# Kernel tuning notes

Hardware: AMD Instinct MI355X
Metric: run time of the kernel (lower is better)

The kernel has to match this reference:

```python
import jax, jax.numpy as jnp
import numpy as np

N = 8_388_608
T_MAX = 4096


def setup_inputs() -> dict:
    key = jax.random.key(0)
    k1, k2, k3 = jax.random.split(key, 3)
    risk = jax.random.normal(k1, (N,), dtype=jnp.float32)
    time = jax.random.randint(k2, (N,), 0, T_MAX, dtype=jnp.int64)
    event = jax.random.randint(k3, (N,), 0, 2, dtype=jnp.int64)
    return {"risk": risk, "time": time, "event": event}


def reference(risk, time, event):
    # Sort descending by time (matches torch.argsort(time, descending=True)).
    order = jnp.argsort(-time)
    r = risk[order]            # [N] risk sorted by descending time
    t = time[order]            # [N]
    e = event[order] > 0       # [N] bool

    n = r.shape[0]
    # Cumulative (prefix) logsumexp over descending-sorted risks.
    # At-risk set for time t is exactly the prefix ending at the LAST index
    # of t's tie group, so log_denom(group) = clse[last_idx_of_group].
    clse = jax.lax.associative_scan(jnp.logaddexp, r)  # [N]

    # Last index of each contiguous tie block (times equal => contiguous after sort).
    is_last = jnp.concatenate([t[:-1] != t[1:], jnp.ones((1,), dtype=bool)])
    idx = jnp.arange(n)
    cand = jnp.where(is_last, idx, n)          # non-last positions -> sentinel
    last_idx = jax.lax.cummin(cand, axis=0, reverse=True)  # min over j >= i

    log_denom = clse[last_idx]                 # [N] per-sample group denominator

    # nll = -sum_groups(sum_{events in group} risk  -  d_group * log_denom)
    #     =  sum_{i: event_i} (log_denom_i - risk_i)
    nll = jnp.sum(jnp.where(e, log_denom - r, jnp.float32(0.0)))

    has_events = jnp.sum(event > 0) > 0
    return jnp.where(has_events, nll, jnp.float32(0.0))
```

## Files before the change

### kernel.cpp

```cpp
#include <hip/hip_runtime.h>

#define TMAX 4096
#define ABLOCKS 256
#define ATHREADS 1024
#define PERTHREAD_V4 8

#define SCALE_F 131072.0f
#define INV_SCALE (1.0 / 131072.0)
#define LSUM_MASK 0x03FFFFFFu
#define LCNT_SHIFT 26
#define LSUM_CAP 67108863.0f

#define SUM_MASK 0xFFFFFFFFFFFFULL
#define CNT_SHIFT 48

#define EVR_SCALE 1048576.0
#define EVR_INV   (1.0 / 1048576.0)

#define PROC1(rv, tv, ev)                                                     \
    do {                                                                      \
        const float xs = fminf(__expf(rv) * SCALE_F + 0.5f, LSUM_CAP);        \
        const unsigned pk = (unsigned)xs                                      \
            | ((unsigned)(ev) << LCNT_SHIFT);                                 \
        atomicAdd(&s_acc[(tv) & (TMAX - 1)], pk);                             \
        evr = __builtin_fmaf((float)(ev), (rv), evr);                         \
    } while (0)

#define PROC4(rr, tt, ee)                                                     \
    do {                                                                      \
        PROC1((rr).x, (tt).x, (ee).x);                                        \
        PROC1((rr).y, (tt).y, (ee).y);                                        \
        PROC1((rr).z, (tt).z, (ee).z);                                        \
        PROC1((rr).w, (tt).w, (ee).w);                                        \
    } while (0)

__global__ __launch_bounds__(ATHREADS, 4) void coxph_fused(
    const float* __restrict__ risk, const int* __restrict__ time_,
    const int* __restrict__ event,
    unsigned long long* __restrict__ gaccR,
    unsigned long long* __restrict__ evracc,
    unsigned* __restrict__ done, float* __restrict__ out)
{
    __shared__ unsigned s_acc[TMAX];
    __shared__ float s_evr[ATHREADS / 64];
    __shared__ unsigned s_old;

    const int tid = threadIdx.x;
    #pragma unroll
    for (int k = 0; k < TMAX / ATHREADS; ++k) s_acc[tid + k * ATHREADS] = 0u;
    __syncthreads();

    const float4* r4 = (const float4*)risk;
    const int4*   t4 = (const int4*)time_;
    const int4*   e4 = (const int4*)event;

    const int base = blockIdx.x * ATHREADS + tid;
    const int S4   = ABLOCKS * ATHREADS;

    float evr = 0.f;

    float4 rA, rB; int4 tA, tB, eA, eB;
#define LOADA(k) do { const int i = base + (k) * S4; rA = r4[i]; tA = t4[i]; eA = e4[i]; } while (0)
#define LOADB(k) do { const int i = base + (k) * S4; rB = r4[i]; tB = t4[i]; eB = e4[i]; } while (0)

    LOADA(0); LOADB(1);
    PROC4(rA, tA, eA); LOADA(2);
    PROC4(rB, tB, eB); LOADB(3);
    PROC4(rA, tA, eA); LOADA(4);
    PROC4(rB, tB, eB); LOADB(5);
    PROC4(rA, tA, eA); LOADA(6);
    PROC4(rB, tB, eB); LOADB(7);
    PROC4(rA, tA, eA);
    PROC4(rB, tB, eB);
#undef LOADA
#undef LOADB

    #pragma unroll
    for (int off = 32; off > 0; off >>= 1) evr += __shfl_down(evr, off);
    const int lane = tid & 63, wave = tid >> 6;
    if (lane == 0) s_evr[wave] = evr;
    __syncthreads();

    #pragma unroll
    for (int k = 0; k < TMAX / ATHREADS; ++k) {
        const int i = tid + k * ATHREADS;
        const unsigned v = s_acc[i];
        if (v) {
            const unsigned long long pk =
                (unsigned long long)(v & LSUM_MASK)
                | ((unsigned long long)(v >> LCNT_SHIFT) << CNT_SHIFT);
            atomicAdd(&gaccR[TMAX - 1 - i], pk);
        }
    }
    if (tid == 0) {
        float tot = 0.f;
        for (int w = 0; w < ATHREADS / 64; ++w) tot += s_evr[w];
        const long long q = (long long)llrint((double)tot * EVR_SCALE);
        atomicAdd(evracc, (unsigned long long)q);
    }

    __syncthreads();
    if (tid == 0) s_old = atomicAdd(done, 1u);
    __syncthreads();
    if (s_old != (unsigned)(ABLOCKS - 1)) return;

    __shared__ float    s_wsum[16];
    __shared__ double   s_dacc[16];
    __shared__ unsigned s_cacc[16];

    const int j0 = 4 * tid;
    const unsigned long long gx = atomicAdd(&gaccR[j0 + 0], 0ull);
    const unsigned long long gy = atomicAdd(&gaccR[j0 + 1], 0ull);
    const unsigned long long gz = atomicAdd(&gaccR[j0 + 2], 0ull);
    const unsigned long long gw = atomicAdd(&gaccR[j0 + 3], 0ull);

    const float v0 = (float)((double)(gx & SUM_MASK) * INV_SCALE);
    const float v1 = (float)((double)(gy & SUM_MASK) * INV_SCALE);
    const float v2 = (float)((double)(gz & SUM_MASK) * INV_SCALE);
    const float v3 = (float)((double)(gw & SUM_MASK) * INV_SCALE);
    const unsigned c0 = (unsigned)(gx >> CNT_SHIFT);
    const unsigned c1 = (unsigned)(gy >> CNT_SHIFT);
    const unsigned c2 = (unsigned)(gz >> CNT_SHIFT);
    const unsigned c3 = (unsigned)(gw >> CNT_SHIFT);

    const float p0 = v0, p1 = p0 + v1, p2 = p1 + v2, p3 = p2 + v3;

    float t_incl = p3;
    #pragma unroll
    for (int off = 1; off < 64; off <<= 1) {
        float u = __shfl_up(t_incl, off);
        if (lane >= off) t_incl += u;
    }
    if (lane == 63) s_wsum[wave] = t_incl;
    __syncthreads();
    if (tid == 0) {
        float a = 0.f;
        for (int w = 0; w < 16; ++w) { float x = s_wsum[w]; s_wsum[w] = a; a += x; }
    }
    __syncthreads();
    const float excl = (t_incl - p3) + s_wsum[wave];

    double acc = 0.0; unsigned ctot = 0u;
    if (c0) { acc += (double)c0 * (double)logf(excl + p0); ctot += c0; }
    if (c1) { acc += (double)c1 * (double)logf(excl + p1); ctot += c1; }
    if (c2) { acc += (double)c2 * (double)logf(excl + p2); ctot += c2; }
    if (c3) { acc += (double)c3 * (double)logf(excl + p3); ctot += c3; }

    if (tid == 0) {
        const long long q = (long long)atomicAdd(evracc, 0ull);
        acc -= (double)q * EVR_INV;
    }

    #pragma unroll
    for (int off = 32; off > 0; off >>= 1) {
        acc  += __shfl_down(acc, off);
        ctot += __shfl_down(ctot, off);
    }
    if (lane == 0) { s_dacc[wave] = acc; s_cacc[wave] = ctot; }
    __syncthreads();
    if (tid == 0) {
        double a = 0.0; unsigned cc = 0u;
        for (int w = 0; w < 16; ++w) { a += s_dacc[w]; cc += s_cacc[w]; }
        out[0] = cc ? (float)a : 0.0f;
    }
}

__global__ __launch_bounds__(ATHREADS, 4) void coxph_hist_generic(
    const float* __restrict__ risk, const int* __restrict__ time_,
    const int* __restrict__ event,
    unsigned long long* __restrict__ gaccR, float* __restrict__ pevr, int n)
{
    __shared__ unsigned long long s_acc[TMAX];
    __shared__ float s_evr[ATHREADS / 64];

    const int tid = threadIdx.x;
    #pragma unroll
    for (int k = 0; k < TMAX / ATHREADS; ++k) s_acc[tid + k * ATHREADS] = 0ull;
    __syncthreads();

    float evr = 0.f;
    const int stride = gridDim.x * ATHREADS;
    for (int i = blockIdx.x * ATHREADS + tid; i < n; i += stride) {
        const float rv = risk[i];
        const int   ev = event[i];
        const int   tv = time_[i];
        const unsigned long long pk =
            (unsigned long long)(unsigned)(__expf(rv) * SCALE_F + 0.5f)
            | ((unsigned long long)(unsigned)ev << CNT_SHIFT);
        atomicAdd(&s_acc[tv & (TMAX - 1)], pk);
        evr = __builtin_fmaf((float)ev, rv, evr);
    }

    #pragma unroll
    for (int off = 32; off > 0; off >>= 1) evr += __shfl_down(evr, off);
    const int lane = tid & 63, wave = tid >> 6;
    if (lane == 0) s_evr[wave] = evr;
    __syncthreads();

    #pragma unroll
    for (int k = 0; k < TMAX / ATHREADS; ++k) {
        const int i = tid + k * ATHREADS;
        const unsigned long long v = s_acc[i];
        if (v) atomicAdd(&gaccR[TMAX - 1 - i], v);
    }
    if (tid == 0) {
        float tot = 0.f;
        for (int w = 0; w < ATHREADS / 64; ++w) tot += s_evr[w];
        pevr[blockIdx.x] = tot;
    }
}

__global__ __launch_bounds__(1024) void coxph_finalize(
    const unsigned long long* __restrict__ gaccR,
    const float* __restrict__ pevr, int nevr, float* __restrict__ out)
{
    __shared__ float    s_wsum[16];
    __shared__ double   s_dacc[16];
    __shared__ unsigned s_cacc[16];

    const int tid = threadIdx.x;
    const int lane = tid & 63, wave = tid >> 6;

    const ulonglong4 g = ((const ulonglong4*)gaccR)[tid];
    const float v0 = (float)((double)(g.x & SUM_MASK) * INV_SCALE);
    const float v1 = (float)((double)(g.y & SUM_MASK) * INV_SCALE);
    const float v2 = (float)((double)(g.z & SUM_MASK) * INV_SCALE);
    const float v3 = (float)((double)(g.w & SUM_MASK) * INV_SCALE);
    const unsigned c0 = (unsigned)(g.x >> CNT_SHIFT);
    const unsigned c1 = (unsigned)(g.y >> CNT_SHIFT);
    const unsigned c2 = (unsigned)(g.z >> CNT_SHIFT);
    const unsigned c3 = (unsigned)(g.w >> CNT_SHIFT);

    const float p0 = v0, p1 = p0 + v1, p2 = p1 + v2, p3 = p2 + v3;

    float t_incl = p3;
    #pragma unroll
    for (int off = 1; off < 64; off <<= 1) {
        float u = __shfl_up(t_incl, off);
        if (lane >= off) t_incl += u;
    }
    if (lane == 63) s_wsum[wave] = t_incl;
    __syncthreads();
    if (tid == 0) {
        float a = 0.f;
        for (int w = 0; w < 16; ++w) { float x = s_wsum[w]; s_wsum[w] = a; a += x; }
    }
    __syncthreads();
    const float excl = (t_incl - p3) + s_wsum[wave];

    double acc = 0.0; unsigned ctot = 0u;
    if (c0) { acc += (double)c0 * (double)logf(excl + p0); ctot += c0; }
    if (c1) { acc += (double)c1 * (double)logf(excl + p1); ctot += c1; }
    if (c2) { acc += (double)c2 * (double)logf(excl + p2); ctot += c2; }
    if (c3) { acc += (double)c3 * (double)logf(excl + p3); ctot += c3; }

    if (tid < nevr) acc -= (double)pevr[tid];

    #pragma unroll
    for (int off = 32; off > 0; off >>= 1) {
        acc  += __shfl_down(acc, off);
        ctot += __shfl_down(ctot, off);
    }
    if (lane == 0) { s_dacc[wave] = acc; s_cacc[wave] = ctot; }
    __syncthreads();
    if (tid == 0) {
        double a = 0.0; unsigned cc = 0u;
        for (int w = 0; w < 16; ++w) { a += s_dacc[w]; cc += s_cacc[w]; }
        out[0] = cc ? (float)a : 0.0f;
    }
}

extern "C" void kernel_launch(void* const* d_in, const int* in_sizes, int n_in,
                              void* d_out, int out_size, void* d_ws, size_t ws_size,
                              hipStream_t stream)
{
    const float* risk  = (const float*)d_in[0];
    const int*   time_ = (const int*)d_in[1];
    const int*   event = (const int*)d_in[2];
    float* out = (float*)d_out;
    const int n = in_sizes[0];

    char* ws = (char*)d_ws;
    unsigned long long* gaccR  = (unsigned long long*)ws;
    unsigned long long* evracc = (unsigned long long*)(ws + TMAX * 8);
    unsigned*           done   = (unsigned*)(ws + TMAX * 8 + 8);
    float*              pevr   = (float*)(ws + TMAX * 8 + 16);

    (void)hipMemsetAsync(ws, 0, TMAX * 8 + 16, stream);

    if (n == ABLOCKS * ATHREADS * 4 * PERTHREAD_V4) {
        coxph_fused<<<ABLOCKS, ATHREADS, 0, stream>>>(
            risk, time_, event, gaccR, evracc, done, out);
    } else {
        coxph_hist_generic<<<ABLOCKS, ATHREADS, 0, stream>>>(
            risk, time_, event, gaccR, pevr, n);
        coxph_finalize<<<1, 1024, 0, stream>>>(gaccR, pevr, ABLOCKS, out);
    }
}
```

Before: 124.2 us.

## Use atomic ticket-based dynamic chunk scheduling in fused CoxPH histogram kernel

```diff
diff --git a/kernel.cpp b/kernel.cpp
--- a/kernel.cpp
+++ b/kernel.cpp
@@ -4,6 +4,9 @@
 #define ABLOCKS 256
 #define ATHREADS 1024
 #define PERTHREAD_V4 8
+
+#define NCHUNK  1024
+#define CHUNKV4 2048
 
 #define SCALE_F 131072.0f
 #define INV_SCALE (1.0 / 131072.0)
@@ -39,46 +42,52 @@
     const int* __restrict__ event,
     unsigned long long* __restrict__ gaccR,
     unsigned long long* __restrict__ evracc,
-    unsigned* __restrict__ done, float* __restrict__ out)
+    unsigned* __restrict__ done, unsigned* __restrict__ ticket,
+    float* __restrict__ out)
 {
     __shared__ unsigned s_acc[TMAX];
-    __shared__ float s_evr[ATHREADS / 64];
+    __shared__ long long s_evrq[ATHREADS / 64];
+    __shared__ unsigned s_chunkbuf[2];
     __shared__ unsigned s_old;
 
     const int tid = threadIdx.x;
+    const int lane = tid & 63, wave = tid >> 6;
+
     #pragma unroll
     for (int k = 0; k < TMAX / ATHREADS; ++k) s_acc[tid + k * ATHREADS] = 0u;
+
+    if (tid == 0) s_chunkbuf[0] = atomicAdd(ticket, 1u);
     __syncthreads();
 
     const float4* r4 = (const float4*)risk;
     const int4*   t4 = (const int4*)time_;
     const int4*   e4 = (const int4*)event;
 
-    const int base = blockIdx.x * ATHREADS + tid;
-    const int S4   = ABLOCKS * ATHREADS;
-
-    float evr = 0.f;
-
-    float4 rA, rB; int4 tA, tB, eA, eB;
-#define LOADA(k) do { const int i = base + (k) * S4; rA = r4[i]; tA = t4[i]; eA = e4[i]; } while (0)
-#define LOADB(k) do { const int i = base + (k) * S4; rB = r4[i]; tB = t4[i]; eB = e4[i]; } while (0)
-
-    LOADA(0); LOADB(1);
-    PROC4(rA, tA, eA); LOADA(2);
-    PROC4(rB, tB, eB); LOADB(3);
-    PROC4(rA, tA, eA); LOADA(4);
-    PROC4(rB, tB, eB); LOADB(5);
-    PROC4(rA, tA, eA); LOADA(6);
-    PROC4(rB, tB, eB); LOADB(7);
-    PROC4(rA, tA, eA);
-    PROC4(rB, tB, eB);
-#undef LOADA
-#undef LOADB
-
-    #pragma unroll
-    for (int off = 32; off > 0; off >>= 1) evr += __shfl_down(evr, off);
-    const int lane = tid & 63, wave = tid >> 6;
-    if (lane == 0) s_evr[wave] = evr;
+    long long evrq = 0;
+    int p = 0;
+    for (;;) {
+        const unsigned c = s_chunkbuf[p];
+        if (tid == 0 && c < NCHUNK)
+            s_chunkbuf[p ^ 1] = atomicAdd(ticket, 1u);
+        if (c >= NCHUNK) break;
+
+        const int vb = (int)c * CHUNKV4 + tid;
+        float4 rA = r4[vb];          int4 tA = t4[vb];          int4 eA = e4[vb];
+        float4 rB = r4[vb + 1024];   int4 tB = t4[vb + 1024];   int4 eB = e4[vb + 1024];
+
+        float evr = 0.f;
+        PROC4(rA, tA, eA);
+        PROC4(rB, tB, eB);
+        evrq += __double2ll_rn((double)evr * EVR_SCALE);
+
+        __syncthreads();
+        p ^= 1;
+    }
+
+    long long q = evrq;
+    #pragma unroll
+    for (int off = 32; off > 0; off >>= 1) q += __shfl_down(q, off);
+    if (lane == 0) s_evrq[wave] = q;
     __syncthreads();
 
     #pragma unroll
@@ -93,10 +102,9 @@
         }
     }
     if (tid == 0) {
-        float tot = 0.f;
-        for (int w = 0; w < ATHREADS / 64; ++w) tot += s_evr[w];
-        const long long q = (long long)llrint((double)tot * EVR_SCALE);
-        atomicAdd(evracc, (unsigned long long)q);
+        long long t = 0;
+        for (int w = 0; w < ATHREADS / 64; ++w) t += s_evrq[w];
+        atomicAdd(evracc, (unsigned long long)t);
     }
 
     __syncthreads();
@@ -147,8 +155,8 @@
     if (c3) { acc += (double)c3 * (double)logf(excl + p3); ctot += c3; }
 
     if (tid == 0) {
-        const long long q = (long long)atomicAdd(evracc, 0ull);
-        acc -= (double)q * EVR_INV;
+        const long long qq = (long long)atomicAdd(evracc, 0ull);
+        acc -= (double)qq * EVR_INV;
     }
 
     #pragma unroll
@@ -284,13 +292,14 @@
     unsigned long long* gaccR  = (unsigned long long*)ws;
     unsigned long long* evracc = (unsigned long long*)(ws + TMAX * 8);
     unsigned*           done   = (unsigned*)(ws + TMAX * 8 + 8);
+    unsigned*           ticket = (unsigned*)(ws + TMAX * 8 + 12);
     float*              pevr   = (float*)(ws + TMAX * 8 + 16);
 
     (void)hipMemsetAsync(ws, 0, TMAX * 8 + 16, stream);
 
     if (n == ABLOCKS * ATHREADS * 4 * PERTHREAD_V4) {
         coxph_fused<<<ABLOCKS, ATHREADS, 0, stream>>>(
-            risk, time_, event, gaccR, evracc, done, out);
+            risk, time_, event, gaccR, evracc, done, ticket, out);
     } else {
         coxph_hist_generic<<<ABLOCKS, ATHREADS, 0, stream>>>(
             risk, time_, event, gaccR, pevr, n);
```

New measurement: 128.4 us. 3.4% more time.
